# Performance work log

Measured on AMD Instinct MI355X. Metric: run time of the kernel, lower is better.

Reference implementation:

```python
import jax, jax.numpy as jnp
import numpy as np
import math

N_HEAD, D_MODEL, D_K, D_V = 8, 512, 64, 64
B, S = 4, 2048
EPS = 1e-5

def _xavier(key, shape):
    fan_in, fan_out = shape
    a = math.sqrt(6.0 / (fan_in + fan_out))
    return jax.random.uniform(key, shape, jnp.float32, -a, a)

def setup_inputs() -> dict:
    key = jax.random.key(0)
    ks = jax.random.split(key, 8)
    q = jax.random.normal(ks[0], (B, S, D_MODEL), jnp.float32)
    k = jax.random.normal(ks[1], (B, S, D_MODEL), jnp.float32)
    v = jax.random.normal(ks[2], (B, S, D_MODEL), jnp.float32)
    mask = jax.random.uniform(ks[3], (B, S, S)) < 0.1
    w_q = _xavier(ks[4], (D_MODEL, N_HEAD * D_K))
    w_k = _xavier(ks[5], (D_MODEL, N_HEAD * D_K))
    w_v = _xavier(ks[6], (D_MODEL, N_HEAD * D_V))
    w_o = _xavier(ks[7], (D_MODEL, N_HEAD * D_V))
    ln_g = jnp.ones((D_MODEL,), jnp.float32)
    ln_b = jnp.zeros((D_MODEL,), jnp.float32)
    return {"q": q, "k": k, "v": v, "w_q": w_q, "w_k": w_k, "w_v": w_v,
            "w_o": w_o, "ln_g": ln_g, "ln_b": ln_b, "mask": mask}

def reference(q, k, v, w_q, w_k, w_v, w_o, ln_g, ln_b, mask):
    b, lq, _ = q.shape
    lk = k.shape[1]
    residual = q
    # projections + head split: [b, len, H, d] -> [b, H, len, d]
    qh = (q @ w_q).reshape(b, lq, N_HEAD, D_K).transpose(0, 2, 1, 3)
    kh = (k @ w_k).reshape(b, lk, N_HEAD, D_K).transpose(0, 2, 1, 3)
    vh = (v @ w_v).reshape(b, lk, N_HEAD, D_V).transpose(0, 2, 1, 3)
    scale = math.sqrt(D_K)
    attn = jnp.einsum('bhqd,bhkd->bhqk', qh, kh) / scale
    attn = jnp.where(mask[:, None, :, :], jnp.float32(-1e9), attn)
    attn = jax.nn.softmax(attn, axis=-1)  # dropout is identity in eval
    heads = jnp.einsum('bhqk,bhkd->bhqd', attn, vh)
    heads = heads.transpose(0, 2, 1, 3).reshape(b, lq, N_HEAD * D_V)
    out = heads @ w_o + residual
    mu = out.mean(-1, keepdims=True)
    var = ((out - mu) ** 2).mean(-1, keepdims=True)
    out = (out - mu) * jax.lax.rsqrt(var + EPS) * ln_g + ln_b
    return out, attn
```

## Files before the change

### kernel.cpp

```cpp
#include <hip/hip_runtime.h>
#include <cstddef>

typedef __attribute__((ext_vector_type(8))) short bf16x8;
typedef __attribute__((ext_vector_type(4))) float f32x4;
typedef __attribute__((ext_vector_type(2))) float f32x2;
typedef __attribute__((ext_vector_type(4))) short short4v;
typedef unsigned long long u64;
typedef unsigned int u32;
typedef unsigned short u16;

#define MFMA16 __builtin_amdgcn_mfma_f32_16x16x32_bf16
static constexpr float LN_EPS = 1e-5f;
static constexpr float L2E = 1.44269504f;

__device__ __forceinline__ u16 f2bf(float f) {
    u32 u = __builtin_bit_cast(u32, f);
    return (u16)((u + 0x7FFFu + ((u >> 16) & 1u)) >> 16);
}
__device__ __forceinline__ float bf2f(u16 h) {
    u32 u = ((u32)h) << 16;
    return __builtin_bit_cast(float, u);
}

__device__ __forceinline__ float block_sum256(float v) {
    __shared__ float sc[4];
    #pragma unroll
    for (int o = 32; o > 0; o >>= 1) v += __shfl_down(v, o);
    if ((threadIdx.x & 63) == 0) sc[threadIdx.x >> 6] = v;
    __syncthreads();
    v = sc[0] + sc[1] + sc[2] + sc[3];
    __syncthreads();
    return v;
}

__global__ __launch_bounds__(256) void prepw_kernel(
    const float* __restrict__ wq, const float* __restrict__ wk,
    const float* __restrict__ wv, const float* __restrict__ wo,
    u16* __restrict__ wt)
{
    const int mat = blockIdx.z;
    const float* W = mat == 0 ? wq : mat == 1 ? wk : mat == 2 ? wv : wo;
    const int k0 = blockIdx.x * 64, n0 = blockIdx.y * 64;
    __shared__ u16 ld[64][72];
    const int t = threadIdx.x;
    {
        const int kk = t >> 2;
        #pragma unroll
        for (int j = 0; j < 4; ++j) {
            const int nn = ((t & 3) + j * 4) * 4;
            float4 x = *(const float4*)&W[(size_t)(k0 + kk) * 512 + n0 + nn];
            ld[kk][nn + 0] = f2bf(x.x); ld[kk][nn + 1] = f2bf(x.y);
            ld[kk][nn + 2] = f2bf(x.z); ld[kk][nn + 3] = f2bf(x.w);
        }
    }
    __syncthreads();
    {
        const int n = t & 63, kc = (t >> 6) * 16;
        u16* op = wt + ((size_t)mat * 512 + n0 + n) * 512 + k0 + kc;
        #pragma unroll
        for (int j = 0; j < 4; ++j) {
            short4v v;
            v[0] = ld[kc + j*4 + 0][n]; v[1] = ld[kc + j*4 + 1][n];
            v[2] = ld[kc + j*4 + 2][n]; v[3] = ld[kc + j*4 + 3][n];
            *(short4v*)(op + j * 4) = v;
        }
    }
}

__global__ __launch_bounds__(256) void prepm_kernel(
    const int* __restrict__ mask, u64* __restrict__ bits)
{
    const int t = threadIdx.x;
    const int row = blockIdx.x * 4 + (t >> 6);
    const int wl = t & 63;
    const int* mrow = mask + (size_t)row * 2048;
    u64* brow = bits + (size_t)row * 32;
    #pragma unroll 8
    for (int it = 0; it < 32; ++it) {
        u64 b = __ballot(mrow[it * 64 + wl] != 0);
        if (wl == 0) brow[it] = b;
    }
}

__global__ __launch_bounds__(256) void proj_kernel(
    const float* __restrict__ qin, const float* __restrict__ kin, const float* __restrict__ vin,
    const u16* __restrict__ wt,
    u16* __restrict__ Qh, u16* __restrict__ Kh, u16* __restrict__ Vt)
{
    const int z = blockIdx.z;
    const float* X = z == 0 ? qin : (z == 1 ? kin : vin);
    const u16* W = wt + (size_t)z * 512 * 512;
    const int m0 = blockIdx.x * 64;
    const int h = blockIdx.y;
    const int t = threadIdx.x, l = t & 63, w = t >> 6;
    const int q = l & 15, G = l >> 4;
    const int wr = w >> 1, wc = w & 1;

    f32x4 acc[2][2] = {};
    for (int k0 = 0; k0 < 512; k0 += 32) {
        bf16x8 af[2], bfr[2];
        #pragma unroll
        for (int mi = 0; mi < 2; ++mi) {
            const float* xp = X + (size_t)(m0 + wr*32 + mi*16 + q) * 512 + k0 + G*8;
            float4 x0 = *(const float4*)xp;
            float4 x1 = *(const float4*)(xp + 4);
            bf16x8 a;
            a[0] = f2bf(x0.x); a[1] = f2bf(x0.y); a[2] = f2bf(x0.z); a[3] = f2bf(x0.w);
            a[4] = f2bf(x1.x); a[5] = f2bf(x1.y); a[6] = f2bf(x1.z); a[7] = f2bf(x1.w);
            af[mi] = a;
        }
        #pragma unroll
        for (int tn = 0; tn < 2; ++tn)
            bfr[tn] = *(const bf16x8*)(W + (size_t)(h*64 + wc*32 + tn*16 + q) * 512 + k0 + G*8);
        #pragma unroll
        for (int mi = 0; mi < 2; ++mi)
            #pragma unroll
            for (int tn = 0; tn < 2; ++tn)
                acc[mi][tn] = MFMA16(af[mi], bfr[tn], acc[mi][tn], 0, 0, 0);
    }
    if (z == 2) {
        #pragma unroll
        for (int mi = 0; mi < 2; ++mi)
            #pragma unroll
            for (int tn = 0; tn < 2; ++tn) {
                const int d = wc*32 + tn*16 + q;
                const int m = m0 + wr*32 + mi*16 + G*4;
                const int bb = m >> 11, s = m & 2047;
                short4v sv;
                #pragma unroll
                for (int r = 0; r < 4; ++r) sv[r] = (short)f2bf(acc[mi][tn][r]);
                *(short4v*)&Vt[(((size_t)(bb*8 + h) << 6) + d) * 2048 + s] = sv;
            }
    } else {
        u16* O = z == 0 ? Qh : Kh;
        const float scv = (z == 0) ? 0.125f : 1.0f;
        #pragma unroll
        for (int mi = 0; mi < 2; ++mi)
            #pragma unroll
            for (int tn = 0; tn < 2; ++tn)
                #pragma unroll
                for (int r = 0; r < 4; ++r) {
                    const int m = m0 + wr*32 + mi*16 + G*4 + r;
                    const int bb = m >> 11, s = m & 2047;
                    const int d = wc*32 + tn*16 + q;
                    O[(((size_t)(bb*8 + h) << 11) + s) * 64 + d] = f2bf(acc[mi][tn][r] * scv);
                }
    }
}

__global__ __launch_bounds__(256) void attnpv_kernel(
    const u16* __restrict__ Qh, const u16* __restrict__ Kh, const u16* __restrict__ Vt,
    const u64* __restrict__ bits,
    float* __restrict__ attn, u16* __restrict__ heads)
{
    const int j   = blockIdx.x;
    const int lid = (j & 7) * 128 + (j >> 3);
    const int qt = lid & 31, bh = lid >> 5;
    const int b = bh >> 3, h = bh & 7;
    const int m0 = qt * 64;
    const int t = threadIdx.x, l = t & 63, w = t >> 6;
    const int q = l & 15, G = l >> 4;
    const int qrow = m0 + w*16 + q;
    __shared__ u16 kbuf[2][4096];
    __shared__ u16 vbuf[2][4096];
    __shared__ u16 alds2[4][2048];
    __shared__ float sinv[64];
    u16* alds2w = alds2[w];

    const size_t qbase = (((size_t)bh << 11) + qrow) * 64;
    bf16x8 qf0 = *(const bf16x8*)(Qh + qbase + G*8);
    bf16x8 qf1 = *(const bf16x8*)(Qh + qbase + 32 + G*8);
    const u64* brow = bits + (((size_t)b << 11) + qrow) * 32;
    const int swz = (q & 7) << 3;

    const int srow0 = t >> 3;
    const int scol  = (t & 7) * 8;
    const u16* Kbase = Kh + (((size_t)bh << 11) * 64);
    const u16* Vbase = Vt + (((size_t)bh << 6) * 2048);
    const int eswz = (t * 8) ^ ((srow0 & 7) << 3);

    bf16x8 sk0, sk1, sv0, sv1;
    float rs = 0.f;

    {
        const u16* kp = Kbase + (size_t)srow0 * 64 + scol;
        sk0 = *(const bf16x8*)kp;
        sk1 = *(const bf16x8*)(kp + 32 * 64);
        *(bf16x8*)&kbuf[0][eswz]        = sk0;
        *(bf16x8*)&kbuf[0][2048 + eswz] = sk1;
    }
    __syncthreads();
    for (int kt = 0; kt < 32; ++kt) {
        const int cur = kt & 1;
        if (kt < 31) {
            const u16* kp = Kbase + (size_t)((kt + 1) * 64 + srow0) * 64 + scol;
            sk0 = *(const bf16x8*)kp;
            sk1 = *(const bf16x8*)(kp + 32 * 64);
        }
        f32x4 acc[4] = {};
        #pragma unroll
        for (int mt = 0; mt < 4; ++mt) {
            const int r = mt*16 + q;
            const int rsw = (r & 7) << 3;
            bf16x8 k0 = *(const bf16x8*)&kbuf[cur][(r*64 +      G*8) ^ rsw];
            bf16x8 k1 = *(const bf16x8*)&kbuf[cur][(r*64 + 32 + G*8) ^ rsw];
            acc[mt] = MFMA16(k0, qf0, acc[mt], 0, 0, 0);
            acc[mt] = MFMA16(k1, qf1, acc[mt], 0, 0, 0);
        }
        const u64 mw = brow[kt];
        #pragma unroll
        for (int mt = 0; mt < 4; ++mt)
            #pragma unroll
            for (int r = 0; r < 4; ++r) {
                const int c = mt*16 + G*4 + r;
                rs += ((mw >> c) & 1) ? 0.f : exp2f(acc[mt][r] * L2E);
            }
        if (kt < 31) {
            *(bf16x8*)&kbuf[cur ^ 1][eswz]        = sk0;
            *(bf16x8*)&kbuf[cur ^ 1][2048 + eswz] = sk1;
        }
        __syncthreads();
    }
    rs += __shfl_xor(rs, 16);
    rs += __shfl_xor(rs, 32);
    const float inv = 1.0f / rs;
    if (G == 0) sinv[w*16 + q] = inv;
    __syncthreads();

    f32x4 pacc[4] = {};
    {
        const u16* kp = Kbase + (size_t)srow0 * 64 + scol;
        sk0 = *(const bf16x8*)kp;
        sk1 = *(const bf16x8*)(kp + 32 * 64);
        const u16* vp = Vbase + (size_t)srow0 * 2048 + scol;
        sv0 = *(const bf16x8*)vp;
        sv1 = *(const bf16x8*)(vp + 32 * 2048);
        *(bf16x8*)&kbuf[0][eswz]        = sk0;
        *(bf16x8*)&kbuf[0][2048 + eswz] = sk1;
        *(bf16x8*)&vbuf[0][eswz]        = sv0;
        *(bf16x8*)&vbuf[0][2048 + eswz] = sv1;
    }
    __syncthreads();
    for (int kt = 0; kt < 32; ++kt) {
        const int cur = kt & 1;
        if (kt < 31) {
            const int n1 = (kt + 1) * 64;
            const u16* kp = Kbase + (size_t)(n1 + srow0) * 64 + scol;
            sk0 = *(const bf16x8*)kp;
            sk1 = *(const bf16x8*)(kp + 32 * 64);
            const u16* vp = Vbase + (size_t)srow0 * 2048 + n1 + scol;
            sv0 = *(const bf16x8*)vp;
            sv1 = *(const bf16x8*)(vp + 32 * 2048);
        }
        f32x4 acc[4] = {};
        #pragma unroll
        for (int mt = 0; mt < 4; ++mt) {
            const int r = mt*16 + q;
            const int rsw = (r & 7) << 3;
            bf16x8 k0 = *(const bf16x8*)&kbuf[cur][(r*64 +      G*8) ^ rsw];
            bf16x8 k1 = *(const bf16x8*)&kbuf[cur][(r*64 + 32 + G*8) ^ rsw];
            acc[mt] = MFMA16(k0, qf0, acc[mt], 0, 0, 0);
            acc[mt] = MFMA16(k1, qf1, acc[mt], 0, 0, 0);
        }
        const u64 mw = brow[kt];
        u16* A2 = alds2w + (kt & 1) * 1024;
        #pragma unroll
        for (int mt = 0; mt < 4; ++mt) {
            short4v sv;
            #pragma unroll
            for (int r = 0; r < 4; ++r) {
                const int c = mt*16 + G*4 + r;
                const float e = ((mw >> c) & 1) ? 0.f : exp2f(acc[mt][r] * L2E);
                sv[r] = (short)f2bf(e);
            }
            *(short4v*)&A2[(q*64 + mt*16 + G*4) ^ swz] = sv;
        }
        bf16x8 an0 = *(const bf16x8*)&A2[(q*64 +  0 + G*8) ^ swz];
        bf16x8 an1 = *(const bf16x8*)&A2[(q*64 + 32 + G*8) ^ swz];
        #pragma unroll
        for (int dmt = 0; dmt < 4; ++dmt) {
            const int r = dmt*16 + q;
            const int rsw = (r & 7) << 3;
            bf16x8 v0 = *(const bf16x8*)&vbuf[cur][(r*64 +      G*8) ^ rsw];
            bf16x8 v1 = *(const bf16x8*)&vbuf[cur][(r*64 + 32 + G*8) ^ rsw];
            pacc[dmt] = MFMA16(v0, an0, pacc[dmt], 0, 0, 0);
            pacc[dmt] = MFMA16(v1, an1, pacc[dmt], 0, 0, 0);
        }
        if (kt < 31) {
            const int nxt = cur ^ 1;
            *(bf16x8*)&kbuf[nxt][eswz]        = sk0;
            *(bf16x8*)&kbuf[nxt][2048 + eswz] = sk1;
            *(bf16x8*)&vbuf[nxt][eswz]        = sv0;
            *(bf16x8*)&vbuf[nxt][2048 + eswz] = sv1;
        }
        if (kt & 1) {
            const int ktg = kt >> 1;
            const u16* A2f = alds2w + (l >> 5) * 1024;
            float* awbase = attn + ((((size_t)bh << 11) + m0 + w*16) << 11) + ktg*128 + l*2;
            #pragma unroll
            for (int r = 0; r < 16; ++r) {
                const float iv = sinv[w*16 + r];
                const u32 e2 = *(const u32*)&A2f[(r*64 + (l & 31)*2) ^ ((r & 7) << 3)];
                f32x2 o;
                o[0] = bf2f((u16)(e2 & 0xffffu)) * iv;
                o[1] = bf2f((u16)(e2 >> 16))     * iv;
                *(f32x2*)(awbase + (size_t)r * 2048) = o;
            }
        }
        __syncthreads();
    }
    #pragma unroll
    for (int dmt = 0; dmt < 4; ++dmt) {
        short4v sv;
        #pragma unroll
        for (int r = 0; r < 4; ++r) sv[r] = (short)f2bf(pacc[dmt][r] * inv);
        *(short4v*)&heads[(((size_t)b << 11) + qrow) * 512 + h*64 + dmt*16 + G*4] = sv;
    }
}

__global__ __launch_bounds__(256) void outgemm_kernel(
    const u16* __restrict__ heads, const u16* __restrict__ wt,
    const float* __restrict__ qin, float* __restrict__ out)
{
    const int m0 = blockIdx.x * 64, n0b = blockIdx.y * 64;
    const int t = threadIdx.x, l = t & 63, w = t >> 6;
    const int q = l & 15, G = l >> 4;
    const int wr = w >> 1, wc = w & 1;
    const u16* W = wt + (size_t)3 * 512 * 512;
    f32x4 acc[2][2] = {};
    for (int k0 = 0; k0 < 512; k0 += 32) {
        bf16x8 af[2], bfr[2];
        #pragma unroll
        for (int mi = 0; mi < 2; ++mi)
            af[mi] = *(const bf16x8*)(heads + (size_t)(m0 + wr*32 + mi*16 + q) * 512 + k0 + G*8);
        #pragma unroll
        for (int tn = 0; tn < 2; ++tn)
            bfr[tn] = *(const bf16x8*)(W + (size_t)(n0b + wc*32 + tn*16 + q) * 512 + k0 + G*8);
        #pragma unroll
        for (int mi = 0; mi < 2; ++mi)
            #pragma unroll
            for (int tn = 0; tn < 2; ++tn)
                acc[mi][tn] = MFMA16(af[mi], bfr[tn], acc[mi][tn], 0, 0, 0);
    }
    #pragma unroll
    for (int mi = 0; mi < 2; ++mi)
        #pragma unroll
        for (int r = 0; r < 4; ++r) {
            const int m = m0 + wr*32 + mi*16 + G*4 + r;
            #pragma unroll
            for (int tn = 0; tn < 2; ++tn) {
                const int n = n0b + wc*32 + tn*16 + q;
                out[(size_t)m * 512 + n] = acc[mi][tn][r] + qin[(size_t)m * 512 + n];
            }
        }
}

__global__ __launch_bounds__(256) void ln_kernel(
    float* __restrict__ out, const float* __restrict__ g, const float* __restrict__ be)
{
    const int m = blockIdx.x;
    float* row = out + (size_t)m * 512;
    const int t = threadIdx.x;
    float2 v = ((const float2*)row)[t];
    float s  = block_sum256(v.x + v.y);
    float s2 = block_sum256(v.x * v.x + v.y * v.y);
    const float mu  = s * (1.0f / 512.0f);
    const float var = s2 * (1.0f / 512.0f) - mu * mu;
    const float inv = rsqrtf(var + LN_EPS);
    float2 gg = ((const float2*)g)[t];
    float2 bb = ((const float2*)be)[t];
    float2 r;
    r.x = (v.x - mu) * inv * gg.x + bb.x;
    r.y = (v.y - mu) * inv * gg.y + bb.y;
    ((float2*)row)[t] = r;
}

extern "C" void kernel_launch(void* const* d_in, const int* in_sizes, int n_in,
                              void* d_out, int out_size, void* d_ws, size_t ws_size,
                              hipStream_t stream) {
    const float* q   = (const float*)d_in[0];
    const float* k   = (const float*)d_in[1];
    const float* v   = (const float*)d_in[2];
    const float* wq  = (const float*)d_in[3];
    const float* wk  = (const float*)d_in[4];
    const float* wv  = (const float*)d_in[5];
    const float* wo  = (const float*)d_in[6];
    const float* g   = (const float*)d_in[7];
    const float* be  = (const float*)d_in[8];
    const int*   msk = (const int*)d_in[9];

    float* out  = (float*)d_out;
    float* attn = out + (size_t)4 * 2048 * 512;

    const size_t nQKV = (size_t)32 * 2048 * 64;
    u16* Qh    = (u16*)d_ws;
    u16* Kh    = Qh + nQKV;
    u16* Vt    = Kh + nQKV;
    u16* heads = Vt + nQKV;
    u16* wt    = heads + (size_t)8192 * 512;
    u64* bits  = (u64*)(wt + (size_t)4 * 512 * 512);

    prepw_kernel  <<<dim3(8, 8, 4),    256, 0, stream>>>(wq, wk, wv, wo, wt);
    prepm_kernel  <<<dim3(2048),       256, 0, stream>>>(msk, bits);
    proj_kernel   <<<dim3(128, 8, 3),  256, 0, stream>>>(q, k, v, wt, Qh, Kh, Vt);
    attnpv_kernel <<<dim3(1024),       256, 0, stream>>>(Qh, Kh, Vt, bits, attn, heads);
    outgemm_kernel<<<dim3(128, 8),     256, 0, stream>>>(heads, wt, q, out);
    ln_kernel     <<<dim3(8192),       256, 0, stream>>>(out, g, be);
}
```

Before: 443.7 us.

## Split softmax row-sum pass into separate kernel with 4x Q-row reuse per K tile

Moves the first pass (masked exp row-sum computation) out of the attention kernel into a dedicated rowsum kernel where each wave handles 64 query rows, reusing each loaded K tile across four query groups. The attention kernel then reads precomputed inverse row sums from workspace instead of recomputing QK^T twice. This cuts K tile loads and LDS traffic for the first pass but adds a kernel launch, extra workspace traffic, and a grid of only 256 blocks that may underfill the GPU.

```diff
diff --git a/kernel.cpp b/kernel.cpp
--- a/kernel.cpp
+++ b/kernel.cpp
@@ -148,9 +148,92 @@
     }
 }
 
+__global__ __launch_bounds__(256) void rowsum_kernel(
+    const u16* __restrict__ Qh, const u16* __restrict__ Kh,
+    const u64* __restrict__ bits, float* __restrict__ invs)
+{
+    const int qtg = blockIdx.x;
+    const int bh  = blockIdx.y;
+    const int b = bh >> 3;
+    const int t = threadIdx.x, l = t & 63, w = t >> 6;
+    const int q = l & 15, G = l >> 4;
+    const int rbase = qtg * 256 + w * 64;
+    __shared__ u16 kbuf[2][4096];
+
+    bf16x8 qf[4][2];
+    #pragma unroll
+    for (int qp = 0; qp < 4; ++qp) {
+        const size_t qb = (((size_t)bh << 11) + rbase + qp*16 + q) * 64;
+        qf[qp][0] = *(const bf16x8*)(Qh + qb + G*8);
+        qf[qp][1] = *(const bf16x8*)(Qh + qb + 32 + G*8);
+    }
+    const u64* brow0 = bits + (((size_t)b << 11) + rbase + q) * 32;
+
+    const int srow0 = t >> 3;
+    const int scol  = (t & 7) * 8;
+    const u16* Kbase = Kh + (((size_t)bh << 11) * 64);
+    const int eswz = (t * 8) ^ ((srow0 & 7) << 3);
+
+    bf16x8 sk0, sk1;
+    float rs[4] = {0.f, 0.f, 0.f, 0.f};
+
+    {
+        const u16* kp = Kbase + (size_t)srow0 * 64 + scol;
+        sk0 = *(const bf16x8*)kp;
+        sk1 = *(const bf16x8*)(kp + 32 * 64);
+        *(bf16x8*)&kbuf[0][eswz]        = sk0;
+        *(bf16x8*)&kbuf[0][2048 + eswz] = sk1;
+    }
+    __syncthreads();
+    for (int kt = 0; kt < 32; ++kt) {
+        const int cur = kt & 1;
+        if (kt < 31) {
+            const u16* kp = Kbase + (size_t)((kt + 1) * 64 + srow0) * 64 + scol;
+            sk0 = *(const bf16x8*)kp;
+            sk1 = *(const bf16x8*)(kp + 32 * 64);
+        }
+        bf16x8 kf[4][2];
+        #pragma unroll
+        for (int mt = 0; mt < 4; ++mt) {
+            const int r = mt*16 + q;
+            const int rsw = (r & 7) << 3;
+            kf[mt][0] = *(const bf16x8*)&kbuf[cur][(r*64 +      G*8) ^ rsw];
+            kf[mt][1] = *(const bf16x8*)&kbuf[cur][(r*64 + 32 + G*8) ^ rsw];
+        }
+        #pragma unroll
+        for (int qp = 0; qp < 4; ++qp) {
+            f32x4 acc[4] = {};
+            #pragma unroll
+            for (int mt = 0; mt < 4; ++mt) {
+                acc[mt] = MFMA16(kf[mt][0], qf[qp][0], acc[mt], 0, 0, 0);
+                acc[mt] = MFMA16(kf[mt][1], qf[qp][1], acc[mt], 0, 0, 0);
+            }
+            const u64 mw = brow0[qp * 16 * 32 + kt];
+            #pragma unroll
+            for (int mt = 0; mt < 4; ++mt)
+                #pragma unroll
+                for (int r = 0; r < 4; ++r) {
+                    const int c = mt*16 + G*4 + r;
+                    rs[qp] += ((mw >> c) & 1) ? 0.f : exp2f(acc[mt][r] * L2E);
+                }
+        }
+        if (kt < 31) {
+            *(bf16x8*)&kbuf[cur ^ 1][eswz]        = sk0;
+            *(bf16x8*)&kbuf[cur ^ 1][2048 + eswz] = sk1;
+        }
+        __syncthreads();
+    }
+    #pragma unroll
+    for (int qp = 0; qp < 4; ++qp) {
+        rs[qp] += __shfl_xor(rs[qp], 16);
+        rs[qp] += __shfl_xor(rs[qp], 32);
+        if (G == 0) invs[((size_t)bh << 11) + rbase + qp*16 + q] = 1.0f / rs[qp];
+    }
+}
+
 __global__ __launch_bounds__(256) void attnpv_kernel(
     const u16* __restrict__ Qh, const u16* __restrict__ Kh, const u16* __restrict__ Vt,
-    const u64* __restrict__ bits,
+    const u64* __restrict__ bits, const float* __restrict__ invs,
     float* __restrict__ attn, u16* __restrict__ heads)
 {
     const int j   = blockIdx.x;
@@ -172,6 +255,8 @@
     bf16x8 qf1 = *(const bf16x8*)(Qh + qbase + 32 + G*8);
     const u64* brow = bits + (((size_t)b << 11) + qrow) * 32;
     const int swz = (q & 7) << 3;
+    const float inv = invs[((size_t)bh << 11) + qrow];
+    if (G == 0) sinv[w*16 + q] = inv;
 
     const int srow0 = t >> 3;
     const int scol  = (t & 7) * 8;
@@ -180,54 +265,8 @@
     const int eswz = (t * 8) ^ ((srow0 & 7) << 3);
 
     bf16x8 sk0, sk1, sv0, sv1;
-    float rs = 0.f;
-
-    {
-        const u16* kp = Kbase + (size_t)srow0 * 64 + scol;
-        sk0 = *(const bf16x8*)kp;
-        sk1 = *(const bf16x8*)(kp + 32 * 64);
-        *(bf16x8*)&kbuf[0][eswz]        = sk0;
-        *(bf16x8*)&kbuf[0][2048 + eswz] = sk1;
-    }
-    __syncthreads();
-    for (int kt = 0; kt < 32; ++kt) {
-        const int cur = kt & 1;
-        if (kt < 31) {
-            const u16* kp = Kbase + (size_t)((kt + 1) * 64 + srow0) * 64 + scol;
-            sk0 = *(const bf16x8*)kp;
-            sk1 = *(const bf16x8*)(kp + 32 * 64);
-        }
-        f32x4 acc[4] = {};
-        #pragma unroll
-        for (int mt = 0; mt < 4; ++mt) {
-            const int r = mt*16 + q;
-            const int rsw = (r & 7) << 3;
-            bf16x8 k0 = *(const bf16x8*)&kbuf[cur][(r*64 +      G*8) ^ rsw];
-            bf16x8 k1 = *(const bf16x8*)&kbuf[cur][(r*64 + 32 + G*8) ^ rsw];
-            acc[mt] = MFMA16(k0, qf0, acc[mt], 0, 0, 0);
-            acc[mt] = MFMA16(k1, qf1, acc[mt], 0, 0, 0);
-        }
-        const u64 mw = brow[kt];
-        #pragma unroll
-        for (int mt = 0; mt < 4; ++mt)
-            #pragma unroll
-            for (int r = 0; r < 4; ++r) {
-                const int c = mt*16 + G*4 + r;
-                rs += ((mw >> c) & 1) ? 0.f : exp2f(acc[mt][r] * L2E);
-            }
-        if (kt < 31) {
-            *(bf16x8*)&kbuf[cur ^ 1][eswz]        = sk0;
-            *(bf16x8*)&kbuf[cur ^ 1][2048 + eswz] = sk1;
-        }
-        __syncthreads();
-    }
-    rs += __shfl_xor(rs, 16);
-    rs += __shfl_xor(rs, 32);
-    const float inv = 1.0f / rs;
-    if (G == 0) sinv[w*16 + q] = inv;
-    __syncthreads();
-
     f32x4 pacc[4] = {};
+
     {
         const u16* kp = Kbase + (size_t)srow0 * 64 + scol;
         sk0 = *(const bf16x8*)kp;
@@ -399,11 +438,13 @@
     u16* heads = Vt + nQKV;
     u16* wt    = heads + (size_t)8192 * 512;
     u64* bits  = (u64*)(wt + (size_t)4 * 512 * 512);
+    float* invs = (float*)(bits + (size_t)8192 * 32);
 
     prepw_kernel  <<<dim3(8, 8, 4),    256, 0, stream>>>(wq, wk, wv, wo, wt);
     prepm_kernel  <<<dim3(2048),       256, 0, stream>>>(msk, bits);
     proj_kernel   <<<dim3(128, 8, 3),  256, 0, stream>>>(q, k, v, wt, Qh, Kh, Vt);
-    attnpv_kernel <<<dim3(1024),       256, 0, stream>>>(Qh, Kh, Vt, bits, attn, heads);
+    rowsum_kernel <<<dim3(8, 32),      256, 0, stream>>>(Qh, Kh, bits, invs);
+    attnpv_kernel <<<dim3(1024),       256, 0, stream>>>(Qh, Kh, Vt, bits, invs, attn, heads);
     outgemm_kernel<<<dim3(128, 8),     256, 0, stream>>>(heads, wt, q, out);
     ln_kernel     <<<dim3(8192),       256, 0, stream>>>(out, g, be);
 }
```

Measured after the change: 459.0 us. 3.4% more time.

## Move softmax row-sum pass into a separate mask-packing kernel

Applied to the files above, without the earlier changes.

Attention previously did two passes over K inside the attention kernel: one to compute masked exp row sums, then one to compute probabilities and PV. The row-sum pass now lives in a new kernel that also packs the mask bits. Each block handles 16 rows for all 8 heads of a batch, reusing the packed mask across heads and reading K straight from global memory without LDS staging. The attention kernel then just loads the precomputed inverse sums. The cost is an extra launch, a small global write and read of the inverse sums, and uncached K reads in the new kernel with only 512 blocks.

```diff
diff --git a/kernel.cpp b/kernel.cpp
--- a/kernel.cpp
+++ b/kernel.cpp
@@ -64,21 +64,6 @@
             v[2] = ld[kc + j*4 + 2][n]; v[3] = ld[kc + j*4 + 3][n];
             *(short4v*)(op + j * 4) = v;
         }
-    }
-}
-
-__global__ __launch_bounds__(256) void prepm_kernel(
-    const int* __restrict__ mask, u64* __restrict__ bits)
-{
-    const int t = threadIdx.x;
-    const int row = blockIdx.x * 4 + (t >> 6);
-    const int wl = t & 63;
-    const int* mrow = mask + (size_t)row * 2048;
-    u64* brow = bits + (size_t)row * 32;
-    #pragma unroll 8
-    for (int it = 0; it < 32; ++it) {
-        u64 b = __ballot(mrow[it * 64 + wl] != 0);
-        if (wl == 0) brow[it] = b;
     }
 }
 
@@ -148,9 +133,74 @@
     }
 }
 
+__global__ __launch_bounds__(256) void maskrow_kernel(
+    const int* __restrict__ mask, const u16* __restrict__ Qh, const u16* __restrict__ Kh,
+    u64* __restrict__ bits, float* __restrict__ invs)
+{
+    const int rg = blockIdx.x;
+    const int bb = blockIdx.y;
+    const int rbase = rg * 16;
+    const int t = threadIdx.x, l = t & 63, w = t >> 6;
+    const int q = l & 15, G = l >> 4;
+    __shared__ u64 mbits[16][33];
+
+    #pragma unroll
+    for (int rp = 0; rp < 4; ++rp) {
+        const int r = rp * 4 + w;
+        const int* mrow = mask + ((((size_t)bb << 11) + rbase + r) << 11);
+        u64* brow = bits + ((((size_t)bb << 11) + rbase + r) << 5);
+        #pragma unroll 8
+        for (int it = 0; it < 32; ++it) {
+            u64 bset = __ballot(mrow[it * 64 + l] != 0);
+            if (l == 0) { mbits[r][it] = bset; brow[it] = bset; }
+        }
+    }
+    __syncthreads();
+
+    bf16x8 qf[2][2];
+    #pragma unroll
+    for (int hp = 0; hp < 2; ++hp) {
+        const int bh = bb * 8 + w * 2 + hp;
+        const size_t qb = (((size_t)bh << 11) + rbase + q) * 64;
+        qf[hp][0] = *(const bf16x8*)(Qh + qb + G*8);
+        qf[hp][1] = *(const bf16x8*)(Qh + qb + 32 + G*8);
+    }
+    float rs[2] = {0.f, 0.f};
+    for (int kt = 0; kt < 32; ++kt) {
+        const u64 mw = mbits[q][kt];
+        #pragma unroll
+        for (int hp = 0; hp < 2; ++hp) {
+            const int bh = bb * 8 + w * 2 + hp;
+            f32x4 acc[4] = {};
+            #pragma unroll
+            for (int mt = 0; mt < 4; ++mt) {
+                const size_t kb = ((((size_t)bh << 11) + kt*64 + mt*16 + q) * 64) + G*8;
+                bf16x8 k0 = *(const bf16x8*)(Kh + kb);
+                bf16x8 k1 = *(const bf16x8*)(Kh + kb + 32);
+                acc[mt] = MFMA16(k0, qf[hp][0], acc[mt], 0, 0, 0);
+                acc[mt] = MFMA16(k1, qf[hp][1], acc[mt], 0, 0, 0);
+            }
+            #pragma unroll
+            for (int mt = 0; mt < 4; ++mt)
+                #pragma unroll
+                for (int r = 0; r < 4; ++r) {
+                    const int c = mt*16 + G*4 + r;
+                    rs[hp] += ((mw >> c) & 1) ? 0.f : exp2f(acc[mt][r] * L2E);
+                }
+        }
+    }
+    #pragma unroll
+    for (int hp = 0; hp < 2; ++hp) {
+        rs[hp] += __shfl_xor(rs[hp], 16);
+        rs[hp] += __shfl_xor(rs[hp], 32);
+        const int bh = bb * 8 + w * 2 + hp;
+        if (G == 0) invs[((size_t)bh << 11) + rbase + q] = 1.0f / rs[hp];
+    }
+}
+
 __global__ __launch_bounds__(256) void attnpv_kernel(
     const u16* __restrict__ Qh, const u16* __restrict__ Kh, const u16* __restrict__ Vt,
-    const u64* __restrict__ bits,
+    const u64* __restrict__ bits, const float* __restrict__ invs,
     float* __restrict__ attn, u16* __restrict__ heads)
 {
     const int j   = blockIdx.x;
@@ -172,6 +222,8 @@
     bf16x8 qf1 = *(const bf16x8*)(Qh + qbase + 32 + G*8);
     const u64* brow = bits + (((size_t)b << 11) + qrow) * 32;
     const int swz = (q & 7) << 3;
+    const float inv = invs[((size_t)bh << 11) + qrow];
+    if (G == 0) sinv[w*16 + q] = inv;
 
     const int srow0 = t >> 3;
     const int scol  = (t & 7) * 8;
@@ -180,54 +232,8 @@
     const int eswz = (t * 8) ^ ((srow0 & 7) << 3);
 
     bf16x8 sk0, sk1, sv0, sv1;
-    float rs = 0.f;
-
-    {
-        const u16* kp = Kbase + (size_t)srow0 * 64 + scol;
-        sk0 = *(const bf16x8*)kp;
-        sk1 = *(const bf16x8*)(kp + 32 * 64);
-        *(bf16x8*)&kbuf[0][eswz]        = sk0;
-        *(bf16x8*)&kbuf[0][2048 + eswz] = sk1;
-    }
-    __syncthreads();
-    for (int kt = 0; kt < 32; ++kt) {
-        const int cur = kt & 1;
-        if (kt < 31) {
-            const u16* kp = Kbase + (size_t)((kt + 1) * 64 + srow0) * 64 + scol;
-            sk0 = *(const bf16x8*)kp;
-            sk1 = *(const bf16x8*)(kp + 32 * 64);
-        }
-        f32x4 acc[4] = {};
-        #pragma unroll
-        for (int mt = 0; mt < 4; ++mt) {
-            const int r = mt*16 + q;
-            const int rsw = (r & 7) << 3;
-            bf16x8 k0 = *(const bf16x8*)&kbuf[cur][(r*64 +      G*8) ^ rsw];
-            bf16x8 k1 = *(const bf16x8*)&kbuf[cur][(r*64 + 32 + G*8) ^ rsw];
-            acc[mt] = MFMA16(k0, qf0, acc[mt], 0, 0, 0);
-            acc[mt] = MFMA16(k1, qf1, acc[mt], 0, 0, 0);
-        }
-        const u64 mw = brow[kt];
-        #pragma unroll
-        for (int mt = 0; mt < 4; ++mt)
-            #pragma unroll
-            for (int r = 0; r < 4; ++r) {
-                const int c = mt*16 + G*4 + r;
-                rs += ((mw >> c) & 1) ? 0.f : exp2f(acc[mt][r] * L2E);
-            }
-        if (kt < 31) {
-            *(bf16x8*)&kbuf[cur ^ 1][eswz]        = sk0;
-            *(bf16x8*)&kbuf[cur ^ 1][2048 + eswz] = sk1;
-        }
-        __syncthreads();
-    }
-    rs += __shfl_xor(rs, 16);
-    rs += __shfl_xor(rs, 32);
-    const float inv = 1.0f / rs;
-    if (G == 0) sinv[w*16 + q] = inv;
-    __syncthreads();
-
     f32x4 pacc[4] = {};
+
     {
         const u16* kp = Kbase + (size_t)srow0 * 64 + scol;
         sk0 = *(const bf16x8*)kp;
@@ -399,11 +405,12 @@
     u16* heads = Vt + nQKV;
     u16* wt    = heads + (size_t)8192 * 512;
     u64* bits  = (u64*)(wt + (size_t)4 * 512 * 512);
+    float* invs = (float*)(bits + (size_t)8192 * 32);
 
     prepw_kernel  <<<dim3(8, 8, 4),    256, 0, stream>>>(wq, wk, wv, wo, wt);
-    prepm_kernel  <<<dim3(2048),       256, 0, stream>>>(msk, bits);
     proj_kernel   <<<dim3(128, 8, 3),  256, 0, stream>>>(q, k, v, wt, Qh, Kh, Vt);
-    attnpv_kernel <<<dim3(1024),       256, 0, stream>>>(Qh, Kh, Vt, bits, attn, heads);
+    maskrow_kernel<<<dim3(128, 4),     256, 0, stream>>>(msk, Qh, Kh, bits, invs);
+    attnpv_kernel <<<dim3(1024),       256, 0, stream>>>(Qh, Kh, Vt, bits, invs, attn, heads);
     outgemm_kernel<<<dim3(128, 8),     256, 0, stream>>>(heads, wt, q, out);
     ln_kernel     <<<dim3(8192),       256, 0, stream>>>(out, g, be);
 }
```

Measured after the change: 555.6 us. +25.2%, slower.
